# Performance work log

Measured on AMD Instinct MI355X. Metric: run time of the kernel, lower is better.

The kernel has to match this reference:

```python
import jax, jax.numpy as jnp
import numpy as np

N = 200000   # n+m+p+q
EMB = 32
K = 3
NNZ = 3200000


def _spmm(vals, rows, cols, X):
    # sparse [N,N] @ dense [N,EMB] via gather + segment-sum scatter
    return jax.ops.segment_sum(vals[:, None] * X[cols], rows, num_segments=N)


def setup_inputs() -> dict:
    key = jax.random.key(0)
    k1, k2, k3, k4 = jax.random.split(key, 4)
    A_vals = jax.random.uniform(k1, (NNZ,), dtype=jnp.float32)
    W0 = jax.random.normal(k2, (N, EMB), dtype=jnp.float32) * 0.01
    alpha = jnp.ones((K + 1,), dtype=jnp.float32) / (K + 1)
    A_rows = jax.random.randint(k3, (NNZ,), 0, N, dtype=jnp.int32)
    A_cols = jax.random.randint(k4, (NNZ,), 0, N, dtype=jnp.int32)
    return {"A_vals": A_vals, "W0": W0, "alpha": alpha,
            "A_rows": A_rows, "A_cols": A_cols}


def reference(A_vals, W0, alpha, A_rows, A_cols):
    E = _spmm(A_vals, A_rows, A_cols, W0)  # E0 = A @ W0
    a = jax.nn.softmax(alpha)
    E_final = a[0] * E
    for i in range(K):  # k-hop propagation, weighted accumulation fused
        E = _spmm(A_vals, A_rows, A_cols, E)
        E_final = E_final + a[i + 1] * E
    return E_final
```

## Files before the change

### kernel.cpp

```cpp
#include <hip/hip_runtime.h>

#define EMB 32
#define SCAN_CHUNK 1024
#define BSHIFT 10
#define ROWS_PER_BUCKET 1024
#define TILE 4096
#define PT_THREADS 256
#define PT_ITEMS 16
#define SP_THREADS 1024


__global__ void bucket_hist_kernel(const int* __restrict__ rows, int nnz,
                                   int* __restrict__ bhist, int nb) {
    __shared__ int h[256];
    int t = threadIdx.x;
    h[t] = 0;
    __syncthreads();
    int stride = gridDim.x * blockDim.x;
    for (int i = blockIdx.x * blockDim.x + t; i < nnz; i += stride)
        atomicAdd(&h[rows[i] >> BSHIFT], 1);
    __syncthreads();
    if (t < nb && h[t] > 0) atomicAdd(&bhist[t], h[t]);
}

__global__ void bucket_scan_kernel(const int* __restrict__ bhist, int nb, int nnz,
                                   int* __restrict__ base, int* __restrict__ cursor) {
    __shared__ int lds[256];
    int t = threadIdx.x;
    int s = (t < nb) ? bhist[t] : 0;
    lds[t] = s;
    __syncthreads();
    for (int off = 1; off < 256; off <<= 1) {
        int add = (t >= off) ? lds[t - off] : 0;
        __syncthreads();
        lds[t] += add;
        __syncthreads();
    }
    if (t < nb) {
        int e = lds[t] - s;
        base[t] = e;
        cursor[t] = e;
    }
    if (t == 0) base[nb] = nnz;
}

__global__ __launch_bounds__(PT_THREADS) void partition_kernel(
        const float* __restrict__ vals, const int* __restrict__ rows,
        const int* __restrict__ cols, int nnz, int* __restrict__ cursor,
        int2* __restrict__ pairs_stage, int* __restrict__ rows_stage) {
    __shared__ int h[256], sc[256], delta[256], cur[256];
    __shared__ float s_val[TILE];
    __shared__ int s_col[TILE], s_row[TILE];
    const int t = threadIdx.x;
    const int tile_start = blockIdx.x * TILE;
    const int tile_cnt = min(TILE, nnz - tile_start);
    h[t] = 0;
    __syncthreads();
    float v[PT_ITEMS];
    int c[PT_ITEMS], r[PT_ITEMS], b[PT_ITEMS];
    #pragma unroll
    for (int k = 0; k < PT_ITEMS; ++k) {
        int i = tile_start + t + k * PT_THREADS;
        if (i < nnz) {
            v[k] = vals[i];
            c[k] = cols[i];
            r[k] = rows[i];
            b[k] = r[k] >> BSHIFT;
            atomicAdd(&h[b[k]], 1);
        } else {
            b[k] = -1;
        }
    }
    __syncthreads();
    int own = h[t];
    sc[t] = own;
    __syncthreads();
    for (int off = 1; off < 256; off <<= 1) {
        int add = (t >= off) ? sc[t - off] : 0;
        __syncthreads();
        sc[t] += add;
        __syncthreads();
    }
    int excl = sc[t] - own;
    if (own > 0) {
        int rsv = atomicAdd(&cursor[t], own);
        delta[t] = rsv - excl;
    }
    cur[t] = excl;
    __syncthreads();
    #pragma unroll
    for (int k = 0; k < PT_ITEMS; ++k) {
        if (b[k] >= 0) {
            int rank = atomicAdd(&cur[b[k]], 1);
            s_val[rank] = v[k];
            s_col[rank] = c[k];
            s_row[rank] = r[k];
        }
    }
    __syncthreads();
    for (int i = t; i < tile_cnt; i += PT_THREADS) {
        int rw = s_row[i];
        int bb = rw >> BSHIFT;
        int gpos = delta[bb] + i;
        pairs_stage[gpos] = make_int2(__float_as_int(s_val[i]), s_col[i]);
        rows_stage[gpos] = rw;
    }
}

__global__ __launch_bounds__(SP_THREADS) void bucket_sort_kernel(
        const int2* __restrict__ pairs_stage, const int* __restrict__ rows_stage,
        const int* __restrict__ base, int n, int nnz,
        int* __restrict__ row_ptr, int2* __restrict__ pairs) {
    __shared__ int rh[ROWS_PER_BUCKET];
    __shared__ int rc[ROWS_PER_BUCKET];
    const int bkt = blockIdx.x;
    const int t = threadIdx.x;
    const int row0 = bkt << BSHIFT;
    const int nrows = min(ROWS_PER_BUCKET, n - row0);
    const int i0 = base[bkt], i1 = base[bkt + 1];
    rh[t] = 0;
    __syncthreads();
    for (int i = i0 + t; i < i1; i += SP_THREADS)
        atomicAdd(&rh[rows_stage[i] - row0], 1);
    __syncthreads();
    int own = rh[t];
    for (int off = 1; off < SP_THREADS; off <<= 1) {
        int add = (t >= off) ? rh[t - off] : 0;
        __syncthreads();
        rh[t] += add;
        __syncthreads();
    }
    int excl = rh[t] - own;
    if (t < nrows) row_ptr[row0 + t] = i0 + excl;
    rc[t] = excl;
    if (bkt == 0 && t == 0) row_ptr[n] = nnz;
    __syncthreads();
    for (int i = i0 + t; i < i1; i += SP_THREADS) {
        int2 p = pairs_stage[i];
        int r = rows_stage[i] - row0;
        int pos = i0 + atomicAdd(&rc[r], 1);
        pairs[pos] = p;
    }
}


__global__ void softmax4_kernel(const float* __restrict__ alpha, float* __restrict__ coefs) {
    if (threadIdx.x == 0 && blockIdx.x == 0) {
        float m = fmaxf(fmaxf(alpha[0], alpha[1]), fmaxf(alpha[2], alpha[3]));
        float e0 = __expf(alpha[0] - m), e1 = __expf(alpha[1] - m);
        float e2 = __expf(alpha[2] - m), e3 = __expf(alpha[3] - m);
        float inv = 1.0f / (e0 + e1 + e2 + e3);
        coefs[0] = e0 * inv; coefs[1] = e1 * inv; coefs[2] = e2 * inv; coefs[3] = e3 * inv;
    }
}


template <bool INIT, bool STORE_E>
__global__ __launch_bounds__(256) void spmm_kernel(
        const int* __restrict__ row_ptr, const int2* __restrict__ pairs,
        const float* __restrict__ X, float* __restrict__ Eout,
        float* __restrict__ Efin, const float* __restrict__ coefs,
        int hop, int n) {
    int tid = blockIdx.x * blockDim.x + threadIdx.x;
    int row = tid >> 3;
    if (row >= n) return;
    const int sub = (tid & 7) * 4;
    int j = row_ptr[row];
    const int j1 = row_ptr[row + 1];
    float ax = 0.f, ay = 0.f, az = 0.f, aw = 0.f;

    if ((j & 1) && j < j1) {
        int2 p = pairs[j];
        float v = __int_as_float(p.x);
        const float4 x = *reinterpret_cast<const float4*>(X + (size_t)p.y * EMB + sub);
        ax = fmaf(v, x.x, ax); ay = fmaf(v, x.y, ay);
        az = fmaf(v, x.z, az); aw = fmaf(v, x.w, aw);
        ++j;
    }
    for (; j + 4 <= j1; j += 4) {
        const int4 pa = *reinterpret_cast<const int4*>(pairs + j);
        const int4 pb = *reinterpret_cast<const int4*>(pairs + j + 2);
        const float4 x0 = *reinterpret_cast<const float4*>(X + (size_t)pa.y * EMB + sub);
        const float4 x1 = *reinterpret_cast<const float4*>(X + (size_t)pa.w * EMB + sub);
        const float4 x2 = *reinterpret_cast<const float4*>(X + (size_t)pb.y * EMB + sub);
        const float4 x3 = *reinterpret_cast<const float4*>(X + (size_t)pb.w * EMB + sub);
        const float v0 = __int_as_float(pa.x), v1 = __int_as_float(pa.z);
        const float v2 = __int_as_float(pb.x), v3 = __int_as_float(pb.z);
        ax = fmaf(v0, x0.x, ax); ay = fmaf(v0, x0.y, ay);
        az = fmaf(v0, x0.z, az); aw = fmaf(v0, x0.w, aw);
        ax = fmaf(v1, x1.x, ax); ay = fmaf(v1, x1.y, ay);
        az = fmaf(v1, x1.z, az); aw = fmaf(v1, x1.w, aw);
        ax = fmaf(v2, x2.x, ax); ay = fmaf(v2, x2.y, ay);
        az = fmaf(v2, x2.z, az); aw = fmaf(v2, x2.w, aw);
        ax = fmaf(v3, x3.x, ax); ay = fmaf(v3, x3.y, ay);
        az = fmaf(v3, x3.z, az); aw = fmaf(v3, x3.w, aw);
    }
    for (; j < j1; ++j) {
        int2 p = pairs[j];
        float v = __int_as_float(p.x);
        const float4 x = *reinterpret_cast<const float4*>(X + (size_t)p.y * EMB + sub);
        ax = fmaf(v, x.x, ax); ay = fmaf(v, x.y, ay);
        az = fmaf(v, x.z, az); aw = fmaf(v, x.w, aw);
    }

    const size_t o = (size_t)row * EMB + sub;
    if (STORE_E)
        *reinterpret_cast<float4*>(Eout + o) = make_float4(ax, ay, az, aw);
    const float a = coefs[hop];
    if (INIT) {
        *reinterpret_cast<float4*>(Efin + o) = make_float4(a * ax, a * ay, a * az, a * aw);
    } else {
        float4 f = *reinterpret_cast<const float4*>(Efin + o);
        f.x += a * ax; f.y += a * ay; f.z += a * az; f.w += a * aw;
        *reinterpret_cast<float4*>(Efin + o) = f;
    }
}


__global__ void spmm_atomic_kernel(const float* __restrict__ vals, const int* __restrict__ rows,
                                   const int* __restrict__ cols, int nnz,
                                   const float* __restrict__ X, float* __restrict__ Eout) {
    long long stride = (long long)gridDim.x * blockDim.x;
    long long total = (long long)nnz * 8;
    for (long long t = (long long)blockIdx.x * blockDim.x + threadIdx.x; t < total; t += stride) {
        int i = (int)(t >> 3);
        int sub = ((int)t & 7) * 4;
        float v = vals[i];
        const float4 x = *reinterpret_cast<const float4*>(X + (long long)cols[i] * EMB + sub);
        float* o = Eout + (long long)rows[i] * EMB + sub;
        atomicAdd(o + 0, v * x.x);
        atomicAdd(o + 1, v * x.y);
        atomicAdd(o + 2, v * x.z);
        atomicAdd(o + 3, v * x.w);
    }
}

template <bool INIT>
__global__ void axpy_kernel(const float* __restrict__ E, float* __restrict__ Efin,
                            const float* __restrict__ coefs, int hop, int total4) {
    int i = blockIdx.x * blockDim.x + threadIdx.x;
    if (i >= total4) return;
    float a = coefs[hop];
    float4 e = reinterpret_cast<const float4*>(E)[i];
    if (INIT) {
        reinterpret_cast<float4*>(Efin)[i] = make_float4(a * e.x, a * e.y, a * e.z, a * e.w);
    } else {
        float4 f = reinterpret_cast<float4*>(Efin)[i];
        f.x += a * e.x; f.y += a * e.y; f.z += a * e.z; f.w += a * e.w;
        reinterpret_cast<float4*>(Efin)[i] = f;
    }
}


extern "C" void kernel_launch(void* const* d_in, const int* in_sizes, int n_in,
                              void* d_out, int out_size, void* d_ws, size_t ws_size,
                              hipStream_t stream) {
    const float* A_vals = (const float*)d_in[0];
    const float* W0     = (const float*)d_in[1];
    const float* alpha  = (const float*)d_in[2];
    const int*   A_rows = (const int*)d_in[3];
    const int*   A_cols = (const int*)d_in[4];
    const int nnz = in_sizes[0];
    const int n   = in_sizes[1] / EMB;
    float* Efin = (float*)d_out;

    char* ws = (char*)d_ws;
    size_t off = 0;
    auto alloc = [&](size_t bytes) -> void* {
        void* p = (void*)(ws + off);
        off += (bytes + 255) & ~(size_t)255;
        return p;
    };

    float* Ebuf0 = (float*)alloc((size_t)n * EMB * 4);
    float* Ebuf1 = (float*)alloc((size_t)n * EMB * 4);
    float* coefs = (float*)alloc(4 * sizeof(float));
    int*  row_ptr = (int*)alloc((size_t)(n + 1) * 4);
    int*  bhist   = (int*)alloc(256 * 4);
    int*  base    = (int*)alloc(257 * 4);
    int*  cursor  = (int*)alloc(256 * 4);
    int2* pairs   = (int2*)alloc((size_t)nnz * 8);
    size_t off_csr = off;

    int2* pairs_stage = (int2*)Ebuf0;
    int*  rows_stage  = (int*)Ebuf1;

    const int nb = (n + ROWS_PER_BUCKET - 1) >> BSHIFT;
    const bool use_csr = (ws_size >= off_csr) && (nb <= 256) &&
                         ((size_t)nnz * 8 <= (size_t)n * EMB * 4);

    softmax4_kernel<<<1, 64, 0, stream>>>(alpha, coefs);

    if (use_csr) {
        hipMemsetAsync(bhist, 0, 256 * 4, stream);
        bucket_hist_kernel<<<1024, 256, 0, stream>>>(A_rows, nnz, bhist, nb);
        bucket_scan_kernel<<<1, 256, 0, stream>>>(bhist, nb, nnz, base, cursor);
        partition_kernel<<<(nnz + TILE - 1) / TILE, PT_THREADS, 0, stream>>>(
            A_vals, A_rows, A_cols, nnz, cursor, pairs_stage, rows_stage);
        bucket_sort_kernel<<<nb, SP_THREADS, 0, stream>>>(
            pairs_stage, rows_stage, base, n, nnz, row_ptr, pairs);

        int blocks = (n * 8 + 255) / 256;
        spmm_kernel<true,  true ><<<blocks, 256, 0, stream>>>(row_ptr, pairs, W0,    Ebuf0, Efin, coefs, 0, n);
        spmm_kernel<false, true ><<<blocks, 256, 0, stream>>>(row_ptr, pairs, Ebuf0, Ebuf1, Efin, coefs, 1, n);
        spmm_kernel<false, true ><<<blocks, 256, 0, stream>>>(row_ptr, pairs, Ebuf1, Ebuf0, Efin, coefs, 2, n);
        spmm_kernel<false, false><<<blocks, 256, 0, stream>>>(row_ptr, pairs, Ebuf0, Ebuf1, Efin, coefs, 3, n);
    } else {
        const float* X = W0;
        float* bufs[2] = {Ebuf0, Ebuf1};
        int total4 = n * EMB / 4;
        int ablocks = (total4 + 255) / 256;
        for (int hop = 0; hop < 4; ++hop) {
            float* Eo = bufs[hop & 1];
            hipMemsetAsync(Eo, 0, (size_t)n * EMB * 4, stream);
            spmm_atomic_kernel<<<2048, 256, 0, stream>>>(A_vals, A_rows, A_cols, nnz, X, Eo);
            if (hop == 0)
                axpy_kernel<true ><<<ablocks, 256, 0, stream>>>(Eo, Efin, coefs, hop, total4);
            else
                axpy_kernel<false><<<ablocks, 256, 0, stream>>>(Eo, Efin, coefs, hop, total4);
            X = Eo;
        }
    }
}
```

Before: 477.1 us.

## Fold bucket scan into partition/sort kernels and pack local row into column bits

Removes the separate bucket_scan kernel launch by having each partition and sort block recompute the 256-entry prefix sum of the bucket histogram locally, with cursors zeroed by an extended memset. The local row index is packed into the upper bits of the column word, shrinking LDS usage in partition. The staged row array becomes 16-bit, cutting staging traffic. Each block now does redundant scan work, and the packing requires n to fit in 18 bits, which is added as a condition for the CSR path.

```diff
diff --git a/kernel.cpp b/kernel.cpp
--- a/kernel.cpp
+++ b/kernel.cpp
@@ -1,18 +1,19 @@
 #include <hip/hip_runtime.h>
 
 #define EMB 32
-#define SCAN_CHUNK 1024
 #define BSHIFT 10
-#define ROWS_PER_BUCKET 1024
+#define RPB 1024
+#define NB 256
 #define TILE 4096
 #define PT_THREADS 256
 #define PT_ITEMS 16
 #define SP_THREADS 1024
+#define COLMASK 0x3FFFF
 
 
 __global__ void bucket_hist_kernel(const int* __restrict__ rows, int nnz,
                                    int* __restrict__ bhist, int nb) {
-    __shared__ int h[256];
+    __shared__ int h[NB];
     int t = threadIdx.x;
     h[t] = 0;
     __syncthreads();
@@ -23,123 +24,131 @@
     if (t < nb && h[t] > 0) atomicAdd(&bhist[t], h[t]);
 }
 
-__global__ void bucket_scan_kernel(const int* __restrict__ bhist, int nb, int nnz,
-                                   int* __restrict__ base, int* __restrict__ cursor) {
-    __shared__ int lds[256];
-    int t = threadIdx.x;
-    int s = (t < nb) ? bhist[t] : 0;
-    lds[t] = s;
-    __syncthreads();
-    for (int off = 1; off < 256; off <<= 1) {
-        int add = (t >= off) ? lds[t - off] : 0;
-        __syncthreads();
-        lds[t] += add;
-        __syncthreads();
-    }
-    if (t < nb) {
-        int e = lds[t] - s;
-        base[t] = e;
-        cursor[t] = e;
-    }
-    if (t == 0) base[nb] = nnz;
-}
-
 __global__ __launch_bounds__(PT_THREADS) void partition_kernel(
         const float* __restrict__ vals, const int* __restrict__ rows,
-        const int* __restrict__ cols, int nnz, int* __restrict__ cursor,
-        int2* __restrict__ pairs_stage, int* __restrict__ rows_stage) {
-    __shared__ int h[256], sc[256], delta[256], cur[256];
+        const int* __restrict__ cols, int nnz,
+        const int* __restrict__ bhist, int* __restrict__ cursor,
+        int2* __restrict__ pairs_stage, unsigned short* __restrict__ lrow_stage) {
+    __shared__ int locbase[NB];
+    __shared__ int h[NB];
+    __shared__ int sc[NB];
+    __shared__ int delta[NB];
     __shared__ float s_val[TILE];
-    __shared__ int s_col[TILE], s_row[TILE];
+    __shared__ int s_pack[TILE];
+    __shared__ unsigned short s_bkt[TILE];
     const int t = threadIdx.x;
     const int tile_start = blockIdx.x * TILE;
     const int tile_cnt = min(TILE, nnz - tile_start);
+
+    const int ownb = bhist[t];
+    locbase[t] = ownb;
     h[t] = 0;
     __syncthreads();
+    for (int off = 1; off < NB; off <<= 1) {
+        int add = (t >= off) ? locbase[t - off] : 0;
+        __syncthreads();
+        locbase[t] += add;
+        __syncthreads();
+    }
+    const int eb = locbase[t] - ownb;
+
     float v[PT_ITEMS];
-    int c[PT_ITEMS], r[PT_ITEMS], b[PT_ITEMS];
+    int pk[PT_ITEMS], b[PT_ITEMS];
     #pragma unroll
     for (int k = 0; k < PT_ITEMS; ++k) {
         int i = tile_start + t + k * PT_THREADS;
         if (i < nnz) {
+            int r = rows[i];
             v[k] = vals[i];
-            c[k] = cols[i];
-            r[k] = rows[i];
-            b[k] = r[k] >> BSHIFT;
+            pk[k] = cols[i] | ((r & (RPB - 1)) << 18);
+            b[k] = r >> BSHIFT;
             atomicAdd(&h[b[k]], 1);
         } else {
             b[k] = -1;
         }
     }
     __syncthreads();
-    int own = h[t];
+    const int own = h[t];
     sc[t] = own;
     __syncthreads();
-    for (int off = 1; off < 256; off <<= 1) {
+    for (int off = 1; off < NB; off <<= 1) {
         int add = (t >= off) ? sc[t - off] : 0;
         __syncthreads();
         sc[t] += add;
         __syncthreads();
     }
-    int excl = sc[t] - own;
+    const int excl = sc[t] - own;
     if (own > 0) {
-        int rsv = atomicAdd(&cursor[t], own);
-        delta[t] = rsv - excl;
-    }
-    cur[t] = excl;
+        int old = atomicAdd(&cursor[t], own);
+        delta[t] = (eb + old) - excl;
+    }
+    h[t] = excl;
     __syncthreads();
     #pragma unroll
     for (int k = 0; k < PT_ITEMS; ++k) {
         if (b[k] >= 0) {
-            int rank = atomicAdd(&cur[b[k]], 1);
+            int rank = atomicAdd(&h[b[k]], 1);
             s_val[rank] = v[k];
-            s_col[rank] = c[k];
-            s_row[rank] = r[k];
+            s_pack[rank] = pk[k];
+            s_bkt[rank] = (unsigned short)b[k];
         }
     }
     __syncthreads();
     for (int i = t; i < tile_cnt; i += PT_THREADS) {
-        int rw = s_row[i];
-        int bb = rw >> BSHIFT;
+        int bb = s_bkt[i];
         int gpos = delta[bb] + i;
-        pairs_stage[gpos] = make_int2(__float_as_int(s_val[i]), s_col[i]);
-        rows_stage[gpos] = rw;
+        int pk_i = s_pack[i];
+        pairs_stage[gpos] = make_int2(__float_as_int(s_val[i]), pk_i);
+        lrow_stage[gpos] = (unsigned short)(((unsigned)pk_i) >> 18);
     }
 }
 
 __global__ __launch_bounds__(SP_THREADS) void bucket_sort_kernel(
-        const int2* __restrict__ pairs_stage, const int* __restrict__ rows_stage,
-        const int* __restrict__ base, int n, int nnz,
+        const int2* __restrict__ pairs_stage, const unsigned short* __restrict__ lrow_stage,
+        const int* __restrict__ bhist, int n, int nnz,
         int* __restrict__ row_ptr, int2* __restrict__ pairs) {
-    __shared__ int rh[ROWS_PER_BUCKET];
-    __shared__ int rc[ROWS_PER_BUCKET];
+    __shared__ int rh[RPB];
+    __shared__ int rc[RPB];
     const int bkt = blockIdx.x;
     const int t = threadIdx.x;
+
+    if (t < NB) rh[t] = bhist[t];
+    __syncthreads();
+    for (int off = 1; off < NB; off <<= 1) {
+        int add = 0;
+        if (t < NB && t >= off) add = rh[t - off];
+        __syncthreads();
+        if (t < NB) rh[t] += add;
+        __syncthreads();
+    }
+    const int i0 = (bkt > 0) ? rh[bkt - 1] : 0;
+    const int i1 = rh[bkt];
+    __syncthreads();
+
     const int row0 = bkt << BSHIFT;
-    const int nrows = min(ROWS_PER_BUCKET, n - row0);
-    const int i0 = base[bkt], i1 = base[bkt + 1];
+    const int nrows = min(RPB, n - row0);
     rh[t] = 0;
     __syncthreads();
     for (int i = i0 + t; i < i1; i += SP_THREADS)
-        atomicAdd(&rh[rows_stage[i] - row0], 1);
-    __syncthreads();
-    int own = rh[t];
+        atomicAdd(&rh[lrow_stage[i]], 1);
+    __syncthreads();
+    const int own = rh[t];
     for (int off = 1; off < SP_THREADS; off <<= 1) {
         int add = (t >= off) ? rh[t - off] : 0;
         __syncthreads();
         rh[t] += add;
         __syncthreads();
     }
-    int excl = rh[t] - own;
+    const int excl = rh[t] - own;
     if (t < nrows) row_ptr[row0 + t] = i0 + excl;
     rc[t] = excl;
     if (bkt == 0 && t == 0) row_ptr[n] = nnz;
     __syncthreads();
     for (int i = i0 + t; i < i1; i += SP_THREADS) {
         int2 p = pairs_stage[i];
-        int r = rows_stage[i] - row0;
+        int r = lrow_stage[i];
         int pos = i0 + atomicAdd(&rc[r], 1);
-        pairs[pos] = p;
+        pairs[pos] = make_int2(p.x, p.y & COLMASK);
     }
 }
 
@@ -276,29 +285,27 @@
     float* Ebuf1 = (float*)alloc((size_t)n * EMB * 4);
     float* coefs = (float*)alloc(4 * sizeof(float));
     int*  row_ptr = (int*)alloc((size_t)(n + 1) * 4);
-    int*  bhist   = (int*)alloc(256 * 4);
-    int*  base    = (int*)alloc(257 * 4);
-    int*  cursor  = (int*)alloc(256 * 4);
+    int*  bhist   = (int*)alloc(NB * 4);
+    int*  cursor  = (int*)alloc(NB * 4);
     int2* pairs   = (int2*)alloc((size_t)nnz * 8);
     size_t off_csr = off;
 
     int2* pairs_stage = (int2*)Ebuf0;
-    int*  rows_stage  = (int*)Ebuf1;
-
-    const int nb = (n + ROWS_PER_BUCKET - 1) >> BSHIFT;
-    const bool use_csr = (ws_size >= off_csr) && (nb <= 256) &&
+    unsigned short* lrow_stage = (unsigned short*)Ebuf1;
+
+    const int nb = (n + RPB - 1) >> BSHIFT;
+    const bool use_csr = (ws_size >= off_csr) && (nb <= NB) && (n <= COLMASK + 1) &&
                          ((size_t)nnz * 8 <= (size_t)n * EMB * 4);
 
     softmax4_kernel<<<1, 64, 0, stream>>>(alpha, coefs);
 
     if (use_csr) {
-        hipMemsetAsync(bhist, 0, 256 * 4, stream);
+        hipMemsetAsync(bhist, 0, 2 * NB * 4, stream);
         bucket_hist_kernel<<<1024, 256, 0, stream>>>(A_rows, nnz, bhist, nb);
-        bucket_scan_kernel<<<1, 256, 0, stream>>>(bhist, nb, nnz, base, cursor);
         partition_kernel<<<(nnz + TILE - 1) / TILE, PT_THREADS, 0, stream>>>(
-            A_vals, A_rows, A_cols, nnz, cursor, pairs_stage, rows_stage);
+            A_vals, A_rows, A_cols, nnz, bhist, cursor, pairs_stage, lrow_stage);
         bucket_sort_kernel<<<nb, SP_THREADS, 0, stream>>>(
-            pairs_stage, rows_stage, base, n, nnz, row_ptr, pairs);
+            pairs_stage, lrow_stage, bhist, n, nnz, row_ptr, pairs);
 
         int blocks = (n * 8 + 255) / 256;
         spmm_kernel<true,  true ><<<blocks, 256, 0, stream>>>(row_ptr, pairs, W0,    Ebuf0, Efin, coefs, 0, n);
```

Measured after the change: 471.7 us. No clear change (-1.1%).
